# Kernel optimization log

Measured on AMD Instinct MI355X. Metric: run time of the kernel, lower is better.

## Reference

```python
import jax, jax.numpy as jnp
import numpy as np

B, CD, GD, F, H = 8192, 512, 512, 1024, 8
HD = F // H
EPS = 1e-5  # torch LayerNorm default


def _layernorm(x, g, b):
    m = x.mean(-1, keepdims=True)
    v = ((x - m) ** 2).mean(-1, keepdims=True)
    return (x - m) / jnp.sqrt(v + EPS) * g + b


def setup_inputs() -> dict:
    key = jax.random.key(0)
    ks = jax.random.split(key, 24)
    s = lambda fan_in: 1.0 / np.sqrt(fan_in)
    return {
        "cnn_embed": jax.random.normal(ks[0], (B, CD), jnp.float32),
        "gnn_embed": jax.random.normal(ks[1], (B, GD), jnp.float32),
        # projections (torch Linear: y = x @ W.T + b)
        "cnn_w": jax.random.normal(ks[2], (F, CD), jnp.float32) * s(CD),
        "cnn_b": jax.random.normal(ks[3], (F,), jnp.float32) * s(CD),
        "gnn_w": jax.random.normal(ks[4], (F, GD), jnp.float32) * s(GD),
        "gnn_b": jax.random.normal(ks[5], (F,), jnp.float32) * s(GD),
        # layernorms
        "ln1_g": jnp.ones((F,), jnp.float32),
        "ln1_b": jnp.zeros((F,), jnp.float32),
        "ln2_g": jnp.ones((F,), jnp.float32),
        "ln2_b": jnp.zeros((F,), jnp.float32),
        # MultiheadAttention packed in-proj + out-proj
        "attn_in_w": jax.random.normal(ks[6], (3 * F, F), jnp.float32) * s(F),
        "attn_in_b": jnp.zeros((3 * F,), jnp.float32),
        "attn_out_w": jax.random.normal(ks[7], (F, F), jnp.float32) * s(F),
        "attn_out_b": jnp.zeros((F,), jnp.float32),
        # gate MLP: Linear(2F->F) GELU Linear(F->2) Softmax
        "gate_w1": jax.random.normal(ks[8], (F, 2 * F), jnp.float32) * s(2 * F),
        "gate_b1": jnp.zeros((F,), jnp.float32),
        "gate_w2": jax.random.normal(ks[9], (2, F), jnp.float32) * s(F),
        "gate_b2": jnp.zeros((2,), jnp.float32),
        # out_proj: Linear(F->F) GELU (dropout is identity in eval)
        "proj_w": jax.random.normal(ks[10], (F, F), jnp.float32) * s(F),
        "proj_b": jnp.zeros((F,), jnp.float32),
    }


def reference(cnn_embed, gnn_embed, cnn_w, cnn_b, gnn_w, gnn_b,
              ln1_g, ln1_b, ln2_g, ln2_b,
              attn_in_w, attn_in_b, attn_out_w, attn_out_b,
              gate_w1, gate_b1, gate_w2, gate_b2, proj_w, proj_b):
    c = _layernorm(cnn_embed @ cnn_w.T + cnn_b, ln1_g, ln1_b)  # [B,F]
    g = _layernorm(gnn_embed @ gnn_w.T + gnn_b, ln2_g, ln2_b)  # [B,F]
    combined = jnp.stack([c, g], axis=1)  # [B,2,F]

    # self-attention over the 2-token "sequence" (q=k=v=combined)
    qkv = combined @ attn_in_w.T + attn_in_b  # [B,2,3F]
    q, k, v = jnp.split(qkv, 3, axis=-1)
    split_heads = lambda t: t.reshape(B, 2, H, HD).transpose(0, 2, 1, 3)  # [B,H,2,HD]
    q, k, v = split_heads(q), split_heads(k), split_heads(v)
    scores = jnp.einsum("bhqd,bhkd->bhqk", q, k) / np.sqrt(HD)  # [B,H,2,2]
    attn = jax.nn.softmax(scores, axis=-1)
    o = jnp.einsum("bhqk,bhkd->bhqd", attn, v)  # [B,H,2,HD]
    o = o.transpose(0, 2, 1, 3).reshape(B, 2, F)
    attn_out = o @ attn_out_w.T + attn_out_b  # [B,2,F]

    c_attn = attn_out[:, 0]
    g_attn = attn_out[:, 1]
    gate_in = jnp.concatenate([c_attn, g_attn], axis=-1)  # [B,2F]
    gate_h = jax.nn.gelu(gate_in @ gate_w1.T + gate_b1, approximate=False)
    gate_weights = jax.nn.softmax(gate_h @ gate_w2.T + gate_b2, axis=-1)  # [B,2]

    fused = gate_weights[:, 0:1] * c_attn + gate_weights[:, 1:2] * g_attn
    fused = jax.nn.gelu(fused @ proj_w.T + proj_b, approximate=False)  # dropout=eval identity
    return fused, gate_weights
```

## Files before the change

### kernel.cpp

```cpp
#include <hip/hip_runtime.h>
#include <hip/hip_bf16.h>
#include <math.h>

typedef short short8 __attribute__((ext_vector_type(8)));
typedef float floatx4 __attribute__((ext_vector_type(4)));

__device__ __forceinline__ float bf2f(ushort u) {
    union { unsigned int i; float f; } v; v.i = ((unsigned int)u) << 16; return v.f;
}
__device__ __forceinline__ ushort f2bf(float f) {
    union { float f; unsigned int i; } v; v.f = f;
    unsigned int x = v.i;
    unsigned int lsb = (x >> 16) & 1u;
    x += 0x7fffu + lsb;
    return (ushort)(x >> 16);
}
__device__ __forceinline__ float gelu_f(float x) {
    return 0.5f * x * (1.0f + erff(x * 0.7071067811865475f));
}
__device__ __forceinline__ void store_out(ushort* p, float v) { *p = f2bf(v); }
__device__ __forceinline__ void store_out(float* p, float v) { *p = v; }

__global__ __launch_bounds__(256) void cvt4_kernel(const float* __restrict__ in,
                                                   ushort* __restrict__ out, int n) {
    int i = (blockIdx.x * 256 + threadIdx.x) * 4;
    if (i >= n) return;
    float4 v = *(const float4*)(in + i);
    ushort4 o;
    o.x = f2bf(v.x); o.y = f2bf(v.y); o.z = f2bf(v.z); o.w = f2bf(v.w);
    *(ushort4*)(out + i) = o;
}

template<int ACT, typename TOUT>
__global__ __launch_bounds__(256) void gemm_bt(const ushort* __restrict__ A, int lda,
                                               const ushort* __restrict__ W,
                                               const float* __restrict__ bias,
                                               TOUT* __restrict__ C, int ldc,
                                               int M, int N, int K) {
    __shared__ ushort lsA[128 * 32];
    __shared__ ushort lsB[128 * 32];
    const int t = threadIdx.x;
    const int w = t >> 6, l = t & 63;
    const int q = l >> 4, r16 = l & 15;
    const int wm = (w >> 1) * 64, wn = (w & 1) * 64;
    const int m0 = blockIdx.y * 128, n0 = blockIdx.x * 128;

    floatx4 acc[4][4];
#pragma unroll
    for (int i = 0; i < 4; i++)
#pragma unroll
        for (int j = 0; j < 4; j++) acc[i][j] = (floatx4){0.f, 0.f, 0.f, 0.f};

    const int kc = (t & 3) * 8;

    for (int kt = 0; kt < K; kt += 32) {
        __syncthreads();
#pragma unroll
        for (int rr = 0; rr < 2; ++rr) {
            int c = rr * 256 + t;
            int row = c >> 2;
            const ushort* ga = A + (size_t)(m0 + row) * lda + kt + kc;
            const ushort* gb = W + (size_t)(n0 + row) * K + kt + kc;
            __builtin_amdgcn_global_load_lds((const __attribute__((address_space(1))) void*)ga,
                                             (__attribute__((address_space(3))) void*)&lsA[c * 8],
                                             16, 0, 0);
            __builtin_amdgcn_global_load_lds((const __attribute__((address_space(1))) void*)gb,
                                             (__attribute__((address_space(3))) void*)&lsB[c * 8],
                                             16, 0, 0);
        }
        __syncthreads();
        short8 af[4], bfr[4];
#pragma unroll
        for (int i = 0; i < 4; i++) af[i]  = *(const short8*)&lsA[(wm + i * 16 + r16) * 32 + q * 8];
#pragma unroll
        for (int j = 0; j < 4; j++) bfr[j] = *(const short8*)&lsB[(wn + j * 16 + r16) * 32 + q * 8];
#pragma unroll
        for (int i = 0; i < 4; i++)
#pragma unroll
            for (int j = 0; j < 4; j++)
                acc[i][j] = __builtin_amdgcn_mfma_f32_16x16x32_bf16(af[i], bfr[j], acc[i][j], 0, 0, 0);
    }

#pragma unroll
    for (int i = 0; i < 4; i++) {
#pragma unroll
        for (int j = 0; j < 4; j++) {
            int col = n0 + wn + j * 16 + r16;
            float bv = bias[col];
#pragma unroll
            for (int rr = 0; rr < 4; rr++) {
                int row = m0 + wm + i * 16 + q * 4 + rr;
                float v = acc[i][j][rr] + bv;
                if (ACT == 1) v = gelu_f(v);
                store_out(&C[(size_t)row * ldc + col], v);
            }
        }
    }
}

__global__ __launch_bounds__(256) void ln_kernel(ushort* __restrict__ comb,
                                                 const float* __restrict__ g1, const float* __restrict__ b1,
                                                 const float* __restrict__ g2, const float* __restrict__ b2) {
    int row = blockIdx.x;
    int s = row & 1;
    const float* g = s ? g2 : g1;
    const float* bb = s ? b2 : b1;
    ushort* p = comb + (size_t)row * 1024;
    int t = threadIdx.x;
    ushort4 u = *(const ushort4*)(p + t * 4);
    float x0 = bf2f(u.x), x1 = bf2f(u.y), x2 = bf2f(u.z), x3 = bf2f(u.w);
    float sum = x0 + x1 + x2 + x3;
    float ss = x0 * x0 + x1 * x1 + x2 * x2 + x3 * x3;
#pragma unroll
    for (int off = 32; off; off >>= 1) {
        sum += __shfl_xor(sum, off);
        ss  += __shfl_xor(ss, off);
    }
    __shared__ float sm[8];
    int wv = t >> 6, l = t & 63;
    if (l == 0) { sm[wv * 2] = sum; sm[wv * 2 + 1] = ss; }
    __syncthreads();
    sum = sm[0] + sm[2] + sm[4] + sm[6];
    ss  = sm[1] + sm[3] + sm[5] + sm[7];
    float mean = sum * (1.0f / 1024.0f);
    float var  = ss * (1.0f / 1024.0f) - mean * mean;
    float rstd = rsqrtf(var + 1e-5f);
    float4 gv = *(const float4*)(g + t * 4);
    float4 bv = *(const float4*)(bb + t * 4);
    ushort4 o;
    o.x = f2bf((x0 - mean) * rstd * gv.x + bv.x);
    o.y = f2bf((x1 - mean) * rstd * gv.y + bv.y);
    o.z = f2bf((x2 - mean) * rstd * gv.z + bv.z);
    o.w = f2bf((x3 - mean) * rstd * gv.w + bv.w);
    *(ushort4*)(p + t * 4) = o;
}

__global__ __launch_bounds__(256) void attn_kernel(ushort* __restrict__ qkv) {
    int wid = blockIdx.x * 4 + (threadIdx.x >> 6);
    int l = threadIdx.x & 63;
    int b = wid >> 3, h = wid & 7;
    ushort* base0 = qkv + (size_t)(b * 2) * 3072 + h * 128;
    ushort* base1 = base0 + 3072;
    float q0a = bf2f(base0[l]),        q0b = bf2f(base0[l + 64]);
    float q1a = bf2f(base1[l]),        q1b = bf2f(base1[l + 64]);
    float k0a = bf2f(base0[1024 + l]), k0b = bf2f(base0[1024 + l + 64]);
    float k1a = bf2f(base1[1024 + l]), k1b = bf2f(base1[1024 + l + 64]);
    float v0a = bf2f(base0[2048 + l]), v0b = bf2f(base0[2048 + l + 64]);
    float v1a = bf2f(base1[2048 + l]), v1b = bf2f(base1[2048 + l + 64]);
    float p00 = q0a * k0a + q0b * k0b;
    float p01 = q0a * k1a + q0b * k1b;
    float p10 = q1a * k0a + q1b * k0b;
    float p11 = q1a * k1a + q1b * k1b;
#pragma unroll
    for (int off = 32; off; off >>= 1) {
        p00 += __shfl_xor(p00, off);
        p01 += __shfl_xor(p01, off);
        p10 += __shfl_xor(p10, off);
        p11 += __shfl_xor(p11, off);
    }
    const float sc = 0.08838834764831845f;
    p00 *= sc; p01 *= sc; p10 *= sc; p11 *= sc;
    float m0 = fmaxf(p00, p01), m1 = fmaxf(p10, p11);
    float e00 = expf(p00 - m0), e01 = expf(p01 - m0);
    float e10 = expf(p10 - m1), e11 = expf(p11 - m1);
    float i0 = 1.0f / (e00 + e01), i1 = 1.0f / (e10 + e11);
    float a00 = e00 * i0, a01 = e01 * i0;
    float a10 = e10 * i1, a11 = e11 * i1;
    base0[l]      = f2bf(a00 * v0a + a01 * v1a);
    base0[l + 64] = f2bf(a00 * v0b + a01 * v1b);
    base1[l]      = f2bf(a10 * v0a + a11 * v1a);
    base1[l + 64] = f2bf(a10 * v0b + a11 * v1b);
}

__global__ __launch_bounds__(256) void gate2_kernel(const ushort* __restrict__ gate_h,
                                                    const float* __restrict__ w2, const float* __restrict__ b2,
                                                    const ushort* __restrict__ attn_out,
                                                    ushort* __restrict__ fused_pre,
                                                    float* __restrict__ gw_out) {
    int b = blockIdx.x;
    int t = threadIdx.x;
    const ushort* hp = gate_h + (size_t)b * 1024;
    ushort4 u = *(const ushort4*)(hp + t * 4);
    float4 w0 = *(const float4*)(w2 + t * 4);
    float4 w1 = *(const float4*)(w2 + 1024 + t * 4);
    float h0 = bf2f(u.x), h1 = bf2f(u.y), h2 = bf2f(u.z), h3 = bf2f(u.w);
    float p0 = h0 * w0.x + h1 * w0.y + h2 * w0.z + h3 * w0.w;
    float p1 = h0 * w1.x + h1 * w1.y + h2 * w1.z + h3 * w1.w;
#pragma unroll
    for (int off = 32; off; off >>= 1) {
        p0 += __shfl_xor(p0, off);
        p1 += __shfl_xor(p1, off);
    }
    __shared__ float sm[8];
    __shared__ float sgw[2];
    int wv = t >> 6, l = t & 63;
    if (l == 0) { sm[wv * 2] = p0; sm[wv * 2 + 1] = p1; }
    __syncthreads();
    if (t == 0) {
        float d0 = sm[0] + sm[2] + sm[4] + sm[6] + b2[0];
        float d1 = sm[1] + sm[3] + sm[5] + sm[7] + b2[1];
        float mx = fmaxf(d0, d1);
        float e0 = expf(d0 - mx), e1 = expf(d1 - mx);
        float inv = 1.0f / (e0 + e1);
        sgw[0] = e0 * inv; sgw[1] = e1 * inv;
        gw_out[b * 2] = e0 * inv;
        gw_out[b * 2 + 1] = e1 * inv;
    }
    __syncthreads();
    float g0 = sgw[0], g1 = sgw[1];
    const ushort* ca = attn_out + (size_t)b * 2048;
    ushort* fp = fused_pre + (size_t)b * 1024;
    ushort4 uc = *(const ushort4*)(ca + t * 4);
    ushort4 ug = *(const ushort4*)(ca + 1024 + t * 4);
    ushort4 o;
    o.x = f2bf(g0 * bf2f(uc.x) + g1 * bf2f(ug.x));
    o.y = f2bf(g0 * bf2f(uc.y) + g1 * bf2f(ug.y));
    o.z = f2bf(g0 * bf2f(uc.z) + g1 * bf2f(ug.z));
    o.w = f2bf(g0 * bf2f(uc.w) + g1 * bf2f(ug.w));
    *(ushort4*)(fp + t * 4) = o;
}

#define OFF_A_CNN  0u
#define OFF_A_GNN  8388608u
#define OFF_W_CNN  16777216u
#define OFF_W_GNN  17825792u
#define OFF_W_QKV  18874368u
#define OFF_W_AO   25165824u
#define OFF_W_G1   27262976u
#define OFF_W_PJ   31457280u
#define OFF_COMB   33554432u
#define OFF_QKV    67108864u
#define OFF_AO     167772160u

extern "C" void kernel_launch(void* const* d_in, const int* in_sizes, int n_in,
                              void* d_out, int out_size, void* d_ws, size_t ws_size,
                              hipStream_t stream) {
    const float* cnn_embed  = (const float*)d_in[0];
    const float* gnn_embed  = (const float*)d_in[1];
    const float* cnn_w      = (const float*)d_in[2];
    const float* cnn_b      = (const float*)d_in[3];
    const float* gnn_w      = (const float*)d_in[4];
    const float* gnn_b      = (const float*)d_in[5];
    const float* ln1_g      = (const float*)d_in[6];
    const float* ln1_b      = (const float*)d_in[7];
    const float* ln2_g      = (const float*)d_in[8];
    const float* ln2_b      = (const float*)d_in[9];
    const float* attn_in_w  = (const float*)d_in[10];
    const float* attn_in_b  = (const float*)d_in[11];
    const float* attn_out_w = (const float*)d_in[12];
    const float* attn_out_b = (const float*)d_in[13];
    const float* gate_w1    = (const float*)d_in[14];
    const float* gate_b1    = (const float*)d_in[15];
    const float* gate_w2    = (const float*)d_in[16];
    const float* gate_b2    = (const float*)d_in[17];
    const float* proj_w     = (const float*)d_in[18];
    const float* proj_b     = (const float*)d_in[19];

    char* ws = (char*)d_ws;
    ushort* a_cnn  = (ushort*)(ws + OFF_A_CNN);
    ushort* a_gnn  = (ushort*)(ws + OFF_A_GNN);
    ushort* w_cnn  = (ushort*)(ws + OFF_W_CNN);
    ushort* w_gnn  = (ushort*)(ws + OFF_W_GNN);
    ushort* w_qkv  = (ushort*)(ws + OFF_W_QKV);
    ushort* w_ao   = (ushort*)(ws + OFF_W_AO);
    ushort* w_g1   = (ushort*)(ws + OFF_W_G1);
    ushort* w_pj   = (ushort*)(ws + OFF_W_PJ);
    ushort* comb   = (ushort*)(ws + OFF_COMB);
    ushort* qkv    = (ushort*)(ws + OFF_QKV);
    ushort* ao     = (ushort*)(ws + OFF_AO);
    ushort* gate_h    = (ushort*)(ws + OFF_COMB);
    ushort* fused_pre = (ushort*)(ws + OFF_COMB + 16777216u);

    float* out_f  = (float*)d_out;
    float* gw_out = out_f + 8192 * 1024;

    cvt4_kernel<<<4194304 / 1024, 256, 0, stream>>>(cnn_embed, a_cnn, 4194304);
    cvt4_kernel<<<4194304 / 1024, 256, 0, stream>>>(gnn_embed, a_gnn, 4194304);
    cvt4_kernel<<<524288 / 1024, 256, 0, stream>>>(cnn_w, w_cnn, 524288);
    cvt4_kernel<<<524288 / 1024, 256, 0, stream>>>(gnn_w, w_gnn, 524288);
    cvt4_kernel<<<3145728 / 1024, 256, 0, stream>>>(attn_in_w, w_qkv, 3145728);
    cvt4_kernel<<<1048576 / 1024, 256, 0, stream>>>(attn_out_w, w_ao, 1048576);
    cvt4_kernel<<<2097152 / 1024, 256, 0, stream>>>(gate_w1, w_g1, 2097152);
    cvt4_kernel<<<1048576 / 1024, 256, 0, stream>>>(proj_w, w_pj, 1048576);

    dim3 blk(256);
    dim3 g_embed(1024 / 128, 8192 / 128);
    gemm_bt<0, ushort><<<g_embed, blk, 0, stream>>>(a_cnn, 512, w_cnn, cnn_b, comb, 2048, 8192, 1024, 512);
    gemm_bt<0, ushort><<<g_embed, blk, 0, stream>>>(a_gnn, 512, w_gnn, gnn_b, comb + 1024, 2048, 8192, 1024, 512);

    ln_kernel<<<16384, blk, 0, stream>>>(comb, ln1_g, ln1_b, ln2_g, ln2_b);

    dim3 g_qkv(3072 / 128, 16384 / 128);
    gemm_bt<0, ushort><<<g_qkv, blk, 0, stream>>>(comb, 1024, w_qkv, attn_in_b, qkv, 3072, 16384, 3072, 1024);

    attn_kernel<<<16384, blk, 0, stream>>>(qkv);

    dim3 g_ao(1024 / 128, 16384 / 128);
    gemm_bt<0, ushort><<<g_ao, blk, 0, stream>>>(qkv, 3072, w_ao, attn_out_b, ao, 1024, 16384, 1024, 1024);

    dim3 g_g1(1024 / 128, 8192 / 128);
    gemm_bt<1, ushort><<<g_g1, blk, 0, stream>>>(ao, 2048, w_g1, gate_b1, gate_h, 1024, 8192, 1024, 2048);

    gate2_kernel<<<8192, blk, 0, stream>>>(gate_h, gate_w2, gate_b2, ao, fused_pre, gw_out);

    dim3 g_pj(1024 / 128, 8192 / 128);
    gemm_bt<1, float><<<g_pj, blk, 0, stream>>>(fused_pre, 1024, w_pj, proj_b, out_f, 1024, 8192, 1024, 1024);
}
```

Measured before the change: 547.5 us.

## Vectorize GEMM epilogue stores, batch fp32-to-bf16 conversions, widen attention loads

Swaps the MFMA operand order so each lane holds four consecutive output columns, which lets the GEMM epilogue do one float4 bias load and one 4-wide store instead of scalar strided stores. The eight separate fp32-to-bf16 conversion launches become a single kernel that walks a descriptor table, cutting launch overhead. The attention kernel now reads and writes adjacent element pairs as ushort2, so each lane owns a different pair of head dimensions but the dot products are unchanged. Together these aim to reduce memory transactions and per-launch overhead.

Result: no change. 545.4 us (-0.4%).

```diff
diff --git a/kernel.cpp b/kernel.cpp
--- a/kernel.cpp
+++ b/kernel.cpp
@@ -18,17 +18,29 @@
 __device__ __forceinline__ float gelu_f(float x) {
     return 0.5f * x * (1.0f + erff(x * 0.7071067811865475f));
 }
-__device__ __forceinline__ void store_out(ushort* p, float v) { *p = f2bf(v); }
-__device__ __forceinline__ void store_out(float* p, float v) { *p = v; }
-
-__global__ __launch_bounds__(256) void cvt4_kernel(const float* __restrict__ in,
-                                                   ushort* __restrict__ out, int n) {
-    int i = (blockIdx.x * 256 + threadIdx.x) * 4;
-    if (i >= n) return;
-    float4 v = *(const float4*)(in + i);
+__device__ __forceinline__ void store4(ushort* p, float a, float b, float c, float d) {
+    ushort4 o; o.x = f2bf(a); o.y = f2bf(b); o.z = f2bf(c); o.w = f2bf(d);
+    *(ushort4*)p = o;
+}
+__device__ __forceinline__ void store4(float* p, float a, float b, float c, float d) {
+    *(float4*)p = make_float4(a, b, c, d);
+}
+
+struct CvtDesc {
+    const float* in[8];
+    ushort* out[8];
+    int nblk[8];
+};
+__global__ __launch_bounds__(256) void cvt_all_kernel(CvtDesc d) {
+    int b = blockIdx.x;
+    int s = 0;
+    int off = b;
+    while (off >= d.nblk[s]) { off -= d.nblk[s]; s++; }
+    int i = off * 1024 + threadIdx.x * 4;
+    float4 v = *(const float4*)(d.in[s] + i);
     ushort4 o;
     o.x = f2bf(v.x); o.y = f2bf(v.y); o.z = f2bf(v.z); o.w = f2bf(v.w);
-    *(ushort4*)(out + i) = o;
+    *(ushort4*)(d.out[s] + i) = o;
 }
 
 template<int ACT, typename TOUT>
@@ -78,22 +90,22 @@
         for (int i = 0; i < 4; i++)
 #pragma unroll
             for (int j = 0; j < 4; j++)
-                acc[i][j] = __builtin_amdgcn_mfma_f32_16x16x32_bf16(af[i], bfr[j], acc[i][j], 0, 0, 0);
-    }
-
-#pragma unroll
-    for (int i = 0; i < 4; i++) {
-#pragma unroll
-        for (int j = 0; j < 4; j++) {
-            int col = n0 + wn + j * 16 + r16;
-            float bv = bias[col];
-#pragma unroll
-            for (int rr = 0; rr < 4; rr++) {
-                int row = m0 + wm + i * 16 + q * 4 + rr;
-                float v = acc[i][j][rr] + bv;
-                if (ACT == 1) v = gelu_f(v);
-                store_out(&C[(size_t)row * ldc + col], v);
-            }
+                acc[i][j] = __builtin_amdgcn_mfma_f32_16x16x32_bf16(bfr[j], af[i], acc[i][j], 0, 0, 0);
+    }
+
+#pragma unroll
+    for (int j = 0; j < 4; j++) {
+        const int col = n0 + wn + j * 16 + q * 4;
+        const float4 bv = *(const float4*)(bias + col);
+#pragma unroll
+        for (int i = 0; i < 4; i++) {
+            const int row = m0 + wm + i * 16 + r16;
+            float v0 = acc[i][j][0] + bv.x;
+            float v1 = acc[i][j][1] + bv.y;
+            float v2 = acc[i][j][2] + bv.z;
+            float v3 = acc[i][j][3] + bv.w;
+            if (ACT == 1) { v0 = gelu_f(v0); v1 = gelu_f(v1); v2 = gelu_f(v2); v3 = gelu_f(v3); }
+            store4(&C[(size_t)row * ldc + col], v0, v1, v2, v3);
         }
     }
 }
@@ -139,14 +151,20 @@
     int wid = blockIdx.x * 4 + (threadIdx.x >> 6);
     int l = threadIdx.x & 63;
     int b = wid >> 3, h = wid & 7;
-    ushort* base0 = qkv + (size_t)(b * 2) * 3072 + h * 128;
+    ushort* base0 = qkv + (size_t)(b * 2) * 3072 + h * 128 + 2 * l;
     ushort* base1 = base0 + 3072;
-    float q0a = bf2f(base0[l]),        q0b = bf2f(base0[l + 64]);
-    float q1a = bf2f(base1[l]),        q1b = bf2f(base1[l + 64]);
-    float k0a = bf2f(base0[1024 + l]), k0b = bf2f(base0[1024 + l + 64]);
-    float k1a = bf2f(base1[1024 + l]), k1b = bf2f(base1[1024 + l + 64]);
-    float v0a = bf2f(base0[2048 + l]), v0b = bf2f(base0[2048 + l + 64]);
-    float v1a = bf2f(base1[2048 + l]), v1b = bf2f(base1[2048 + l + 64]);
+    ushort2 uq0 = *(const ushort2*)(base0);
+    ushort2 uq1 = *(const ushort2*)(base1);
+    ushort2 uk0 = *(const ushort2*)(base0 + 1024);
+    ushort2 uk1 = *(const ushort2*)(base1 + 1024);
+    ushort2 uv0 = *(const ushort2*)(base0 + 2048);
+    ushort2 uv1 = *(const ushort2*)(base1 + 2048);
+    float q0a = bf2f(uq0.x), q0b = bf2f(uq0.y);
+    float q1a = bf2f(uq1.x), q1b = bf2f(uq1.y);
+    float k0a = bf2f(uk0.x), k0b = bf2f(uk0.y);
+    float k1a = bf2f(uk1.x), k1b = bf2f(uk1.y);
+    float v0a = bf2f(uv0.x), v0b = bf2f(uv0.y);
+    float v1a = bf2f(uv1.x), v1b = bf2f(uv1.y);
     float p00 = q0a * k0a + q0b * k0b;
     float p01 = q0a * k1a + q0b * k1b;
     float p10 = q1a * k0a + q1b * k0b;
@@ -166,10 +184,13 @@
     float i0 = 1.0f / (e00 + e01), i1 = 1.0f / (e10 + e11);
     float a00 = e00 * i0, a01 = e01 * i0;
     float a10 = e10 * i1, a11 = e11 * i1;
-    base0[l]      = f2bf(a00 * v0a + a01 * v1a);
-    base0[l + 64] = f2bf(a00 * v0b + a01 * v1b);
-    base1[l]      = f2bf(a10 * v0a + a11 * v1a);
-    base1[l + 64] = f2bf(a10 * v0b + a11 * v1b);
+    ushort2 o0, o1;
+    o0.x = f2bf(a00 * v0a + a01 * v1a);
+    o0.y = f2bf(a00 * v0b + a01 * v1b);
+    o1.x = f2bf(a10 * v0a + a11 * v1a);
+    o1.y = f2bf(a10 * v0b + a11 * v1b);
+    *(ushort2*)(base0) = o0;
+    *(ushort2*)(base1) = o1;
 }
 
 __global__ __launch_bounds__(256) void gate2_kernel(const ushort* __restrict__ gate_h,
@@ -274,14 +295,16 @@
     float* out_f  = (float*)d_out;
     float* gw_out = out_f + 8192 * 1024;
 
-    cvt4_kernel<<<4194304 / 1024, 256, 0, stream>>>(cnn_embed, a_cnn, 4194304);
-    cvt4_kernel<<<4194304 / 1024, 256, 0, stream>>>(gnn_embed, a_gnn, 4194304);
-    cvt4_kernel<<<524288 / 1024, 256, 0, stream>>>(cnn_w, w_cnn, 524288);
-    cvt4_kernel<<<524288 / 1024, 256, 0, stream>>>(gnn_w, w_gnn, 524288);
-    cvt4_kernel<<<3145728 / 1024, 256, 0, stream>>>(attn_in_w, w_qkv, 3145728);
-    cvt4_kernel<<<1048576 / 1024, 256, 0, stream>>>(attn_out_w, w_ao, 1048576);
-    cvt4_kernel<<<2097152 / 1024, 256, 0, stream>>>(gate_w1, w_g1, 2097152);
-    cvt4_kernel<<<1048576 / 1024, 256, 0, stream>>>(proj_w, w_pj, 1048576);
+    CvtDesc cd;
+    cd.in[0] = cnn_embed;  cd.out[0] = a_cnn; cd.nblk[0] = 4096;
+    cd.in[1] = gnn_embed;  cd.out[1] = a_gnn; cd.nblk[1] = 4096;
+    cd.in[2] = cnn_w;      cd.out[2] = w_cnn; cd.nblk[2] = 512;
+    cd.in[3] = gnn_w;      cd.out[3] = w_gnn; cd.nblk[3] = 512;
+    cd.in[4] = attn_in_w;  cd.out[4] = w_qkv; cd.nblk[4] = 3072;
+    cd.in[5] = attn_out_w; cd.out[5] = w_ao;  cd.nblk[5] = 1024;
+    cd.in[6] = gate_w1;    cd.out[6] = w_g1;  cd.nblk[6] = 2048;
+    cd.in[7] = proj_w;     cd.out[7] = w_pj;  cd.nblk[7] = 1024;
+    cvt_all_kernel<<<16384, 256, 0, stream>>>(cd);
 
     dim3 blk(256);
     dim3 g_embed(1024 / 128, 8192 / 128);
```
